# Kernel tuning notes

Measured on AMD Instinct MI355X. Metric: run time of the kernel, lower is better.

Reference implementation:

```python
import jax, jax.numpy as jnp
import numpy as np

N_QUBITS = 11
N_TOKENS = 32
D_MODEL = 512
DEGREE = 2
N_LAYERS = 1
DIM = 2 ** N_QUBITS
N_PQC = 4 * N_QUBITS * N_LAYERS


def _apply_ry(U, theta, q):
    # left-multiply U by I_{2^q} (x) RY(theta) (x) I_{2^{n-q-1}} without materializing the kron
    c = jnp.cos(theta / 2)
    s = jnp.sin(theta / 2)
    g = jnp.stack([jnp.stack([c, -s]), jnp.stack([s, c])]).astype(jnp.complex64)  # [2,2]
    left = 2 ** q
    Ur = U.reshape(left, 2, DIM // (2 * left), DIM)
    return jnp.einsum('ab,xbyd->xayd', g, Ur).reshape(DIM, DIM)


def _build_unitary(params):
    # Faithful to _build_unitary_matrix_gpu: only RY gates alter U; the CRX helper
    # in the source returns U unchanged (bug preserved), so CRX params are skipped.
    U = jnp.eye(DIM, dtype=jnp.complex64)
    for layer in range(N_LAYERS):
        base = layer * 4 * N_QUBITS
        for block in (0, 2):  # RY blocks at offsets 0 and 2*n; CRX blocks (1,3) are no-ops
            for i in range(N_QUBITS):
                U = _apply_ry(U, params[base + block * N_QUBITS + i], i)
    return U


def _e0():
    return jnp.zeros(DIM, jnp.complex64).at[0].set(1.0)


def _apply_lcu(state, Us, coeffs):
    norm = jnp.linalg.norm(state)
    small = norm < 1e-8
    safe = jnp.where(small, jnp.float32(1.0), norm)
    init = jnp.where(small, _e0(), state / safe)
    evolved = jnp.einsum('tij,j->ti', Us, init)      # [L_limit, dim]
    lcu = jnp.einsum('t,ti->i', coeffs, evolved)     # [dim]
    return jnp.where(small, jnp.float32(1.0), norm) * lcu


def _measure(state, ff_params):
    U_ff = _build_unitary(ff_params)
    st = U_ff @ state
    X = jnp.array([[0, 1], [1, 0]], jnp.complex64)
    Y = jnp.array([[0, -1j], [1j, 0]], jnp.complex64)
    Z = jnp.array([[1, 0], [0, -1]], jnp.complex64)
    exps = []
    for q in range(N_QUBITS):
        sr = st.reshape(2 ** q, 2, -1)
        for P in (X, Y, Z):  # source _measure_on_gpu order: X,Y,Z per qubit
            ps = jnp.einsum('ab,xby->xay', P, sr)
            exps.append(jnp.real(jnp.sum(jnp.conj(sr) * ps)))
    return jnp.stack(exps)  # [3*n_qubits]


def setup_inputs() -> dict:
    key = jax.random.key(0)
    ks = jax.random.split(key, 7)
    return {
        'tokens_emb': jax.random.normal(ks[0], (N_TOKENS, D_MODEL), jnp.float32),
        'W_angles': jax.random.normal(ks[1], (N_PQC, D_MODEL), jnp.float32) * (1.0 / np.sqrt(D_MODEL)),
        'b_angles': jax.random.normal(ks[2], (N_PQC,), jnp.float32) * 0.01,
        'qsvt_coeffs': jax.random.normal(ks[3], (DEGREE + 1,), jnp.float32) * 0.1,
        'lcu_re': jax.random.normal(ks[4], (N_TOKENS,), jnp.float32),
        'lcu_im': jax.random.normal(ks[5], (N_TOKENS,), jnp.float32),
        'ff_params': jax.random.normal(ks[6], (N_PQC,), jnp.float32),
    }


def reference(tokens_emb, W_angles, b_angles, qsvt_coeffs, lcu_re, lcu_im, ff_params):
    L = tokens_emb.shape[0]
    L_used = min(L, N_TOKENS)
    angles = tokens_emb[:L_used] @ W_angles.T + b_angles        # [L_used, n_pqc]
    lcu = (lcu_re + 1j * lcu_im).astype(jnp.complex64)[:L_used]
    lcu = lcu / jnp.clip(jnp.sum(jnp.abs(lcu)), 1e-8)
    L_limit = min(L_used, 4)  # hardcoded in source _apply_lcu_fast
    Us = jax.vmap(_build_unitary)(angles[:L_limit])              # [L_limit, dim, dim]

    e0 = _e0()
    acc = qsvt_coeffs[0] * e0
    monomial = e0
    for k in range(1, DEGREE + 1):
        monomial = _apply_lcu(monomial, Us, lcu[:L_limit])
        acc = acc + qsvt_coeffs[k] * monomial
    poly_norm = jnp.sum(jnp.abs(qsvt_coeffs))
    acc = acc / jnp.clip(poly_norm, 1e-8)

    sn = jnp.linalg.norm(acc)
    small = sn < 1e-8
    safe = jnp.where(small, jnp.float32(1.0), sn)
    ff_in = jnp.where(small, e0, acc / safe)
    return _measure(ff_in, ff_params)
```

## Files before the change

### kernel.cpp

```cpp
#include <hip/hip_runtime.h>
#include <math.h>


#define NQ 11

template<int CTRL>
__device__ __forceinline__ float dpp_mov(float x) {
    return __int_as_float(__builtin_amdgcn_update_dpp(
        0, __float_as_int(x), CTRL, 0xF, 0xF, false));
}

__device__ __forceinline__ float wave_sum(float v) {
    v += dpp_mov<0x111>(v);
    v += dpp_mov<0x112>(v);
    v += dpp_mov<0x114>(v);
    v += dpp_mov<0x118>(v);
    v += dpp_mov<0x142>(v);
    v += dpp_mov<0x143>(v);
    return __int_as_float(__builtin_amdgcn_readlane(__float_as_int(v), 63));
}

#define REG_STAGE(q, m) do {                                                  \
    const float cq_ = C[q], sq_ = S[q];                                       \
    _Pragma("unroll")                                                         \
    for (int r_ = 0; r_ < 32; r_++) {                                         \
        if (!(r_ & (m))) {                                                    \
            const int b_ = r_ | (m);                                          \
            const float axr = sr[r_], axi = si[r_];                           \
            const float bxr = sr[b_], bxi = si[b_];                           \
            sr[r_] = cq_ * axr - sq_ * bxr;                                   \
            si[r_] = cq_ * axi - sq_ * bxi;                                   \
            sr[b_] = sq_ * axr + cq_ * bxr;                                   \
            si[b_] = sq_ * axi + cq_ * bxi;                                   \
        }                                                                     \
    }                                                                         \
} while (0)

#define DPP_STAGE() do {                                                      \
    const float cq_ = C[5];                                                   \
    const float ssn_ = (lane & 1) ? S[5] : -S[5];                             \
    _Pragma("unroll")                                                         \
    for (int r_ = 0; r_ < 32; r_++) {                                         \
        const float pr_ = dpp_mov<0xB1>(sr[r_]);                              \
        const float pi_ = dpp_mov<0xB1>(si[r_]);                              \
        sr[r_] = cq_ * sr[r_] + ssn_ * pr_;                                   \
        si[r_] = cq_ * si[r_] + ssn_ * pi_;                                   \
    }                                                                         \
} while (0)

#define T_A2B() do {                                                          \
    _Pragma("unroll")                                                         \
    for (int r_ = 0; r_ < 32; r_++) {                                         \
        const int i_ = (r_ << 6) | lane;                                      \
        ws[i_ ^ (r_ & 15)] = make_float2(sr[r_], si[r_]);                     \
    }                                                                         \
    __builtin_amdgcn_sched_barrier(0);                                        \
    _Pragma("unroll")                                                         \
    for (int r_ = 0; r_ < 32; r_++) {                                         \
        const float2 v_ = ws[((lane << 5) | r_) ^ ((lane >> 1) & 15)];        \
        sr[r_] = v_.x; si[r_] = v_.y;                                         \
    }                                                                         \
} while (0)

#define T_B2A() do {                                                          \
    _Pragma("unroll")                                                         \
    for (int r_ = 0; r_ < 32; r_++) {                                         \
        ws[((lane << 5) | r_) ^ ((lane >> 1) & 15)] =                         \
            make_float2(sr[r_], si[r_]);                                      \
    }                                                                         \
    __builtin_amdgcn_sched_barrier(0);                                        \
    _Pragma("unroll")                                                         \
    for (int r_ = 0; r_ < 32; r_++) {                                         \
        const float2 v_ = ws[((r_ << 6) | lane) ^ (r_ & 15)];                 \
        sr[r_] = v_.x; si[r_] = v_.y;                                         \
    }                                                                         \
} while (0)

#define APPLY_CORE() do {                                                     \
    REG_STAGE(0, 16); REG_STAGE(1, 8); REG_STAGE(2, 4);                       \
    REG_STAGE(3, 2);  REG_STAGE(4, 1);                                        \
    T_A2B();                                                                  \
    REG_STAGE(6, 16); REG_STAGE(7, 8); REG_STAGE(8, 4);                       \
    REG_STAGE(9, 2);  REG_STAGE(10, 1);                                       \
    DPP_STAGE();                                                              \
} while (0)

#define MEASURE_REGBIT(q, m) do {                                             \
    float px_ = 0.f, py_ = 0.f, pz_ = 0.f;                                    \
    _Pragma("unroll")                                                         \
    for (int r_ = 0; r_ < 32; r_++) {                                         \
        const int j_ = r_ ^ (m);                                              \
        px_ += sr[r_] * sr[j_] + si[r_] * si[j_];                             \
        const float imz_ = sr[r_] * si[j_] - si[r_] * sr[j_];                 \
        py_ += (r_ & (m)) ? -imz_ : imz_;                                     \
        const float p2_ = sr[r_] * sr[r_] + si[r_] * si[r_];                  \
        pz_ += (r_ & (m)) ? -p2_ : p2_;                                       \
    }                                                                         \
    px_ = wave_sum(px_); py_ = wave_sum(py_); pz_ = wave_sum(pz_);            \
    if (lane == 0) {                                                          \
        out[3 * (q) + 0] = px_;                                               \
        out[3 * (q) + 1] = py_;                                               \
        out[3 * (q) + 2] = pz_;                                               \
    }                                                                         \
} while (0)

#define MEASURE_Q5() do {                                                     \
    float px_ = 0.f, py_ = 0.f, pz_ = 0.f;                                    \
    const int bit_ = lane & 1;                                                \
    _Pragma("unroll")                                                         \
    for (int r_ = 0; r_ < 32; r_++) {                                         \
        const float pr_ = dpp_mov<0xB1>(sr[r_]);                              \
        const float pi_ = dpp_mov<0xB1>(si[r_]);                              \
        px_ += sr[r_] * pr_ + si[r_] * pi_;                                   \
        const float imz_ = sr[r_] * pi_ - si[r_] * pr_;                       \
        py_ += bit_ ? -imz_ : imz_;                                           \
        const float p2_ = sr[r_] * sr[r_] + si[r_] * si[r_];                  \
        pz_ += bit_ ? -p2_ : p2_;                                             \
    }                                                                         \
    px_ = wave_sum(px_); py_ = wave_sum(py_); pz_ = wave_sum(pz_);            \
    if (lane == 0) { out[15] = px_; out[16] = py_; out[17] = pz_; }           \
} while (0)

__global__ __launch_bounds__(256, 1) void quixer_kernel(
    const float* __restrict__ emb,
    const float* __restrict__ Wang,
    const float* __restrict__ bang,
    const float* __restrict__ qc,
    const float* __restrict__ lre,
    const float* __restrict__ lim,
    const float* __restrict__ ffp,
    float* __restrict__ out)
{
    __shared__ float2 ex[4][2048];

    const int tid  = threadIdx.x;
    const int w    = tid >> 6;
    const int lane = tid & 63;
    float2* ws = &ex[w][0];

    float C[NQ], S[NQ];
    {
        const float* e = emb + (w << 9);
        float ev[8];
#pragma unroll
        for (int j = 0; j < 8; j++) ev[j] = e[lane + (j << 6)];
        float part[NQ];
#pragma unroll
        for (int q = 0; q < NQ; q++) {
            const float* w0 = Wang + (q << 9);
            const float* w1 = Wang + ((q + 22) << 9);
            float a = 0.f;
#pragma unroll
            for (int j = 0; j < 8; j++) {
                const int d = lane + (j << 6);
                a += ev[j] * (w0[d] + w1[d]);
            }
            part[q] = a;
        }
#pragma unroll
        for (int q = 0; q < NQ; q++) {
            const float phi = wave_sum(part[q]) + bang[q] + bang[q + 22];
            __sincosf(0.5f * phi, &S[q], &C[q]);
        }
    }

    float lr, li;
    {
        float av = 0.f;
        if (lane < 32) {
            const float re = lre[lane], iv = lim[lane];
            av = sqrtf(re * re + iv * iv);
        }
        const float denom = fmaxf(wave_sum(av), 1e-8f);
        lr = lre[w] / denom;
        li = lim[w] / denom;
    }
    const float qc0 = qc[0], qc1 = qc[1], qc2 = qc[2];

    float sr[32], si[32], ar[32], ai[32];
#pragma unroll
    for (int r = 0; r < 32; r++) { sr[r] = 0.f; si[r] = 0.f; ar[r] = 0.f; ai[r] = 0.f; }
    if (lane == 0) { sr[0] = 1.f; ar[0] = qc0; }

#pragma unroll
    for (int k = 1; k <= 2; k++) {
        float nsq = 0.f;
#pragma unroll
        for (int r = 0; r < 32; r++) nsq += sr[r] * sr[r] + si[r] * si[r];
        nsq = wave_sum(nsq);
        if (sqrtf(nsq) < 1e-8f) {
#pragma unroll
            for (int r = 0; r < 32; r++) { sr[r] = 0.f; si[r] = 0.f; }
            if (lane == 0) sr[0] = 1.f;
        }

        APPLY_CORE();
        T_B2A();

#pragma unroll
        for (int r = 0; r < 32; r++) {
            const int i = (r << 6) | lane;
            ws[i] = make_float2(lr * sr[r] - li * si[r],
                                lr * si[r] + li * sr[r]);
        }
        __syncthreads();
#pragma unroll
        for (int r = 0; r < 32; r++) {
            const int i = (r << 6) | lane;
            const float2 v0 = ex[0][i], v1 = ex[1][i], v2 = ex[2][i], v3 = ex[3][i];
            sr[r] = v0.x + v1.x + v2.x + v3.x;
            si[r] = v0.y + v1.y + v2.y + v3.y;
        }
        const float qk = (k == 1) ? qc1 : qc2;
#pragma unroll
        for (int r = 0; r < 32; r++) { ar[r] += qk * sr[r]; ai[r] += qk * si[r]; }
        __syncthreads();
    }

    const float pn = fmaxf(fabsf(qc0) + fabsf(qc1) + fabsf(qc2), 1e-8f);
    float snsq = 0.f;
#pragma unroll
    for (int r = 0; r < 32; r++) snsq += ar[r] * ar[r] + ai[r] * ai[r];
    snsq = wave_sum(snsq);
    if (sqrtf(snsq) / pn < 1e-8f) {
#pragma unroll
        for (int r = 0; r < 32; r++) { sr[r] = 0.f; si[r] = 0.f; }
        if (lane == 0) sr[0] = 1.f;
    } else {
        const float inv = 1.f / sqrtf(snsq);
#pragma unroll
        for (int r = 0; r < 32; r++) { sr[r] = ar[r] * inv; si[r] = ai[r] * inv; }
    }

#pragma unroll
    for (int q = 0; q < NQ; q++) {
        const float phi = ffp[q] + ffp[q + 22];
        __sincosf(0.5f * phi, &S[q], &C[q]);
    }
    APPLY_CORE();

    switch (w) {
        case 0: MEASURE_REGBIT(8, 4);  break;
        case 1: MEASURE_Q5(); MEASURE_REGBIT(9, 2); break;
        case 2: MEASURE_REGBIT(6, 16); MEASURE_REGBIT(10, 1); break;
        case 3: MEASURE_REGBIT(7, 8);  break;
    }
    T_B2A();
    switch (w) {
        case 0: MEASURE_REGBIT(0, 16); MEASURE_REGBIT(4, 1); break;
        case 1: MEASURE_REGBIT(1, 8);  break;
        case 2: MEASURE_REGBIT(2, 4);  break;
        case 3: MEASURE_REGBIT(3, 2);  break;
    }
}

extern "C" void kernel_launch(void* const* d_in, const int* in_sizes, int n_in,
                              void* d_out, int out_size, void* d_ws, size_t ws_size,
                              hipStream_t stream) {
    quixer_kernel<<<1, 256, 0, stream>>>(
        (const float*)d_in[0],
        (const float*)d_in[1],
        (const float*)d_in[2],
        (const float*)d_in[3],
        (const float*)d_in[4],
        (const float*)d_in[5],
        (const float*)d_in[6],
        (float*)d_out);
}
```

Measured before the change: 82.08 us.

## Closed-form first LCU step and packed float2 math for state updates

The first monomial application, which acts on the basis state e0, is replaced by a closed form. Each wave builds column 0 of its RY unitary as a tensor product of cos/sin factors, writes it as real floats to shared memory, and then combines the four columns with the complex LCU coefficients. This removes one full apply-core pass, its transposes and the normalisation check. Separately, the state registers are repacked as two-wide float vectors so the compiler can emit packed FMA instructions in the rotation stages. The risk is register pressure from the extra coefficient arrays, and the closed form relies on the initial state being exactly e0.

```diff
diff --git a/kernel.cpp b/kernel.cpp
--- a/kernel.cpp
+++ b/kernel.cpp
@@ -3,6 +3,9 @@
 
 
 #define NQ 11
+typedef float v2f __attribute__((ext_vector_type(2)));
+
+__device__ __forceinline__ v2f splat(float x) { v2f v; v.x = x; v.y = x; return v; }
 
 template<int CTRL>
 __device__ __forceinline__ float dpp_mov(float x) {
@@ -21,30 +24,27 @@
 }
 
 #define REG_STAGE(q, m) do {                                                  \
-    const float cq_ = C[q], sq_ = S[q];                                       \
+    const v2f cq_ = splat(C[q]), sq_ = splat(S[q]);                           \
     _Pragma("unroll")                                                         \
     for (int r_ = 0; r_ < 32; r_++) {                                         \
         if (!(r_ & (m))) {                                                    \
             const int b_ = r_ | (m);                                          \
-            const float axr = sr[r_], axi = si[r_];                           \
-            const float bxr = sr[b_], bxi = si[b_];                           \
-            sr[r_] = cq_ * axr - sq_ * bxr;                                   \
-            si[r_] = cq_ * axi - sq_ * bxi;                                   \
-            sr[b_] = sq_ * axr + cq_ * bxr;                                   \
-            si[b_] = sq_ * axi + cq_ * bxi;                                   \
+            const v2f a_ = sv[r_], b2_ = sv[b_];                              \
+            sv[r_] = cq_ * a_ - sq_ * b2_;                                    \
+            sv[b_] = sq_ * a_ + cq_ * b2_;                                    \
         }                                                                     \
     }                                                                         \
 } while (0)
 
 #define DPP_STAGE() do {                                                      \
-    const float cq_ = C[5];                                                   \
-    const float ssn_ = (lane & 1) ? S[5] : -S[5];                             \
-    _Pragma("unroll")                                                         \
-    for (int r_ = 0; r_ < 32; r_++) {                                         \
-        const float pr_ = dpp_mov<0xB1>(sr[r_]);                              \
-        const float pi_ = dpp_mov<0xB1>(si[r_]);                              \
-        sr[r_] = cq_ * sr[r_] + ssn_ * pr_;                                   \
-        si[r_] = cq_ * si[r_] + ssn_ * pi_;                                   \
+    const v2f cq_ = splat(C[5]);                                              \
+    const v2f ssn_ = splat((lane & 1) ? S[5] : -S[5]);                        \
+    _Pragma("unroll")                                                         \
+    for (int r_ = 0; r_ < 32; r_++) {                                         \
+        v2f p_;                                                               \
+        p_.x = dpp_mov<0xB1>(sv[r_].x);                                       \
+        p_.y = dpp_mov<0xB1>(sv[r_].y);                                       \
+        sv[r_] = cq_ * sv[r_] + ssn_ * p_;                                    \
     }                                                                         \
 } while (0)
 
@@ -52,13 +52,13 @@
     _Pragma("unroll")                                                         \
     for (int r_ = 0; r_ < 32; r_++) {                                         \
         const int i_ = (r_ << 6) | lane;                                      \
-        ws[i_ ^ (r_ & 15)] = make_float2(sr[r_], si[r_]);                     \
+        ws[i_ ^ (r_ & 15)] = make_float2(sv[r_].x, sv[r_].y);                 \
     }                                                                         \
     __builtin_amdgcn_sched_barrier(0);                                        \
     _Pragma("unroll")                                                         \
     for (int r_ = 0; r_ < 32; r_++) {                                         \
         const float2 v_ = ws[((lane << 5) | r_) ^ ((lane >> 1) & 15)];        \
-        sr[r_] = v_.x; si[r_] = v_.y;                                         \
+        sv[r_].x = v_.x; sv[r_].y = v_.y;                                     \
     }                                                                         \
 } while (0)
 
@@ -66,13 +66,13 @@
     _Pragma("unroll")                                                         \
     for (int r_ = 0; r_ < 32; r_++) {                                         \
         ws[((lane << 5) | r_) ^ ((lane >> 1) & 15)] =                         \
-            make_float2(sr[r_], si[r_]);                                      \
+            make_float2(sv[r_].x, sv[r_].y);                                  \
     }                                                                         \
     __builtin_amdgcn_sched_barrier(0);                                        \
     _Pragma("unroll")                                                         \
     for (int r_ = 0; r_ < 32; r_++) {                                         \
         const float2 v_ = ws[((r_ << 6) | lane) ^ (r_ & 15)];                 \
-        sr[r_] = v_.x; si[r_] = v_.y;                                         \
+        sv[r_].x = v_.x; sv[r_].y = v_.y;                                     \
     }                                                                         \
 } while (0)
 
@@ -90,10 +90,10 @@
     _Pragma("unroll")                                                         \
     for (int r_ = 0; r_ < 32; r_++) {                                         \
         const int j_ = r_ ^ (m);                                              \
-        px_ += sr[r_] * sr[j_] + si[r_] * si[j_];                             \
-        const float imz_ = sr[r_] * si[j_] - si[r_] * sr[j_];                 \
+        px_ += sv[r_].x * sv[j_].x + sv[r_].y * sv[j_].y;                     \
+        const float imz_ = sv[r_].x * sv[j_].y - sv[r_].y * sv[j_].x;         \
         py_ += (r_ & (m)) ? -imz_ : imz_;                                     \
-        const float p2_ = sr[r_] * sr[r_] + si[r_] * si[r_];                  \
+        const float p2_ = sv[r_].x * sv[r_].x + sv[r_].y * sv[r_].y;          \
         pz_ += (r_ & (m)) ? -p2_ : p2_;                                       \
     }                                                                         \
     px_ = wave_sum(px_); py_ = wave_sum(py_); pz_ = wave_sum(pz_);            \
@@ -109,12 +109,12 @@
     const int bit_ = lane & 1;                                                \
     _Pragma("unroll")                                                         \
     for (int r_ = 0; r_ < 32; r_++) {                                         \
-        const float pr_ = dpp_mov<0xB1>(sr[r_]);                              \
-        const float pi_ = dpp_mov<0xB1>(si[r_]);                              \
-        px_ += sr[r_] * pr_ + si[r_] * pi_;                                   \
-        const float imz_ = sr[r_] * pi_ - si[r_] * pr_;                       \
+        const float pr_ = dpp_mov<0xB1>(sv[r_].x);                            \
+        const float pi_ = dpp_mov<0xB1>(sv[r_].y);                            \
+        px_ += sv[r_].x * pr_ + sv[r_].y * pi_;                               \
+        const float imz_ = sv[r_].x * pi_ - sv[r_].y * pr_;                   \
         py_ += bit_ ? -imz_ : imz_;                                           \
-        const float p2_ = sr[r_] * sr[r_] + si[r_] * si[r_];                  \
+        const float p2_ = sv[r_].x * sv[r_].x + sv[r_].y * sv[r_].y;          \
         pz_ += bit_ ? -p2_ : p2_;                                             \
     }                                                                         \
     px_ = wave_sum(px_); py_ = wave_sum(py_); pz_ = wave_sum(pz_);            \
@@ -164,7 +164,7 @@
         }
     }
 
-    float lr, li;
+    float lrv[4], liv[4];
     {
         float av = 0.f;
         if (lane < 32) {
@@ -172,64 +172,103 @@
             av = sqrtf(re * re + iv * iv);
         }
         const float denom = fmaxf(wave_sum(av), 1e-8f);
-        lr = lre[w] / denom;
-        li = lim[w] / denom;
+#pragma unroll
+        for (int t = 0; t < 4; t++) { lrv[t] = lre[t] / denom; liv[t] = lim[t] / denom; }
     }
     const float qc0 = qc[0], qc1 = qc[1], qc2 = qc[2];
 
-    float sr[32], si[32], ar[32], ai[32];
-#pragma unroll
-    for (int r = 0; r < 32; r++) { sr[r] = 0.f; si[r] = 0.f; ar[r] = 0.f; ai[r] = 0.f; }
-    if (lane == 0) { sr[0] = 1.f; ar[0] = qc0; }
-
-#pragma unroll
-    for (int k = 1; k <= 2; k++) {
+    v2f sv[32], av[32];
+#pragma unroll
+    for (int r = 0; r < 32; r++) { av[r].x = 0.f; av[r].y = 0.f; }
+    if (lane == 0) av[0].x = qc0;
+
+    {
+        float lp = 1.f;
+#pragma unroll
+        for (int q = 5; q < 11; q++)
+            lp *= ((lane >> (10 - q)) & 1) ? S[q] : C[q];
+        float t[32];
+        t[0] = lp;
+#pragma unroll
+        for (int q = 4; q >= 0; q--) {
+            const int m = 1 << (4 - q);
+#pragma unroll
+            for (int j = 0; j < 32; j++) {
+                if (j < m) {
+                    t[j | m] = t[j] * S[q];
+                    t[j]     = t[j] * C[q];
+                }
+            }
+        }
+        float* wsf = (float*)ws;
+#pragma unroll
+        for (int r = 0; r < 32; r++) wsf[(r << 6) | lane] = t[r];
+        __syncthreads();
+        const float* exf = (const float*)(&ex[0][0]);
+#pragma unroll
+        for (int r = 0; r < 32; r++) {
+            const int i = (r << 6) | lane;
+            const float v0 = exf[i], v1 = exf[4096 + i];
+            const float v2 = exf[8192 + i], v3 = exf[12288 + i];
+            v2f m0;
+            m0.x = lrv[0]*v0 + lrv[1]*v1 + lrv[2]*v2 + lrv[3]*v3;
+            m0.y = liv[0]*v0 + liv[1]*v1 + liv[2]*v2 + liv[3]*v3;
+            sv[r] = m0;
+            av[r] += splat(qc1) * m0;
+        }
+        __syncthreads();
+    }
+
+    {
         float nsq = 0.f;
 #pragma unroll
-        for (int r = 0; r < 32; r++) nsq += sr[r] * sr[r] + si[r] * si[r];
+        for (int r = 0; r < 32; r++) nsq += sv[r].x * sv[r].x + sv[r].y * sv[r].y;
         nsq = wave_sum(nsq);
         if (sqrtf(nsq) < 1e-8f) {
 #pragma unroll
-            for (int r = 0; r < 32; r++) { sr[r] = 0.f; si[r] = 0.f; }
-            if (lane == 0) sr[0] = 1.f;
+            for (int r = 0; r < 32; r++) { sv[r].x = 0.f; sv[r].y = 0.f; }
+            if (lane == 0) sv[0].x = 1.f;
         }
 
         APPLY_CORE();
         T_B2A();
 
+        const float lr = lrv[w], li = liv[w];
 #pragma unroll
         for (int r = 0; r < 32; r++) {
             const int i = (r << 6) | lane;
-            ws[i] = make_float2(lr * sr[r] - li * si[r],
-                                lr * si[r] + li * sr[r]);
+            ws[i] = make_float2(lr * sv[r].x - li * sv[r].y,
+                                lr * sv[r].y + li * sv[r].x);
         }
         __syncthreads();
 #pragma unroll
         for (int r = 0; r < 32; r++) {
             const int i = (r << 6) | lane;
             const float2 v0 = ex[0][i], v1 = ex[1][i], v2 = ex[2][i], v3 = ex[3][i];
-            sr[r] = v0.x + v1.x + v2.x + v3.x;
-            si[r] = v0.y + v1.y + v2.y + v3.y;
-        }
-        const float qk = (k == 1) ? qc1 : qc2;
-#pragma unroll
-        for (int r = 0; r < 32; r++) { ar[r] += qk * sr[r]; ai[r] += qk * si[r]; }
+            v2f m0;
+            m0.x = v0.x + v1.x + v2.x + v3.x;
+            m0.y = v0.y + v1.y + v2.y + v3.y;
+            sv[r] = m0;
+            av[r] += splat(qc2) * m0;
+        }
         __syncthreads();
     }
 
-    const float pn = fmaxf(fabsf(qc0) + fabsf(qc1) + fabsf(qc2), 1e-8f);
-    float snsq = 0.f;
-#pragma unroll
-    for (int r = 0; r < 32; r++) snsq += ar[r] * ar[r] + ai[r] * ai[r];
-    snsq = wave_sum(snsq);
-    if (sqrtf(snsq) / pn < 1e-8f) {
-#pragma unroll
-        for (int r = 0; r < 32; r++) { sr[r] = 0.f; si[r] = 0.f; }
-        if (lane == 0) sr[0] = 1.f;
-    } else {
-        const float inv = 1.f / sqrtf(snsq);
-#pragma unroll
-        for (int r = 0; r < 32; r++) { sr[r] = ar[r] * inv; si[r] = ai[r] * inv; }
+    {
+        const float pn = fmaxf(fabsf(qc0) + fabsf(qc1) + fabsf(qc2), 1e-8f);
+        float snsq = 0.f;
+#pragma unroll
+        for (int r = 0; r < 32; r++) snsq += av[r].x * av[r].x + av[r].y * av[r].y;
+        snsq = wave_sum(snsq);
+        if (sqrtf(snsq) / pn < 1e-8f) {
+#pragma unroll
+            for (int r = 0; r < 32; r++) { sv[r].x = 0.f; sv[r].y = 0.f; }
+            if (lane == 0) sv[0].x = 1.f;
+        } else {
+            const v2f inv = splat(1.f / sqrtf(snsq));
+#pragma unroll
+            for (int r = 0; r < 32; r++) sv[r] = av[r] * inv;
+        }
     }
 
 #pragma unroll
```

Measured after the change: 81.13 us. Within noise of the previous version (-1.2%).
